# Kernel optimization log

Measured on AMD Instinct MI355X. Metric: run time of the kernel, lower is better.

The kernel has to match this reference:

```python
import jax, jax.numpy as jnp
import numpy as np

B, S, H = 1, 1024, 2048
E, F, FS = 32, 768, 4096
TOP_K = 4
SCALE = 0.02


def setup_inputs() -> dict:
    key = jax.random.key(0)
    ks = jax.random.split(key, 9)
    return {
        "hidden_states": jax.random.normal(ks[0], (B, S, H), jnp.float32),
        "router_weight": jax.random.normal(ks[1], (E, H), jnp.float32) * SCALE,
        "w_gate": jax.random.normal(ks[2], (E, H, F), jnp.float32) * SCALE,
        "w_up": jax.random.normal(ks[3], (E, H, F), jnp.float32) * SCALE,
        "w_down": jax.random.normal(ks[4], (E, F, H), jnp.float32) * SCALE,
        "sw_gate": jax.random.normal(ks[5], (H, FS), jnp.float32) * SCALE,
        "sw_up": jax.random.normal(ks[6], (H, FS), jnp.float32) * SCALE,
        "sw_down": jax.random.normal(ks[7], (FS, H), jnp.float32) * SCALE,
        "sgate_w": jax.random.normal(ks[8], (H, 1), jnp.float32) * SCALE,
    }


def reference(hidden_states, router_weight, w_gate, w_up, w_down,
              sw_gate, sw_up, sw_down, sgate_w):
    b, s, h = hidden_states.shape
    x = hidden_states.reshape(-1, h)                      # [T,H]
    T = x.shape[0]

    # ---- router: linear -> softmax (fp32) -> topk -> renormalize ----
    logits = x @ router_weight.T                          # [T,E]
    probs = jax.nn.softmax(logits.astype(jnp.float32), axis=-1)
    topv, topi = jax.lax.top_k(probs, TOP_K)              # [T,K]
    topv = topv / jnp.sum(topv, axis=-1, keepdims=True)
    topv = topv.astype(probs.dtype)

    # combine weights: scatter topk weights into dense [T,E] mask
    combine = jnp.zeros((T, E), probs.dtype).at[
        jnp.arange(T)[:, None], topi].add(topv)

    # ---- experts: SwiGLU per expert, weighted combine ----
    g = jnp.einsum('th,ehf->etf', x, w_gate)              # [E,T,F]
    u = jnp.einsum('th,ehf->etf', x, w_up)                # [E,T,F]
    act = jax.nn.silu(g) * u                              # [E,T,F]
    out = jnp.einsum('te,etf,efh->th', combine, act, w_down)  # [T,H]

    # ---- shared expert with sigmoid gate ----
    shared = (jax.nn.silu(x @ sw_gate) * (x @ sw_up)) @ sw_down  # [T,H]
    out = out + jax.nn.sigmoid(x @ sgate_w) * shared

    return out.reshape(b, s, h)
```

## Files before the change

kernel.cpp:

```cpp
#include <hip/hip_runtime.h>
#include <math.h>

#define T_TOK 1024
#define H_DIM 2048
#define N_EXP 32
#define TOPK  4
#define F_DIM 768
#define FS_DIM 4096
#define FS_HALF 2048

typedef __bf16 bf16;
typedef __attribute__((ext_vector_type(4))) __bf16 bf16x4;
typedef __attribute__((ext_vector_type(8))) __bf16 bf16x8;
typedef __attribute__((ext_vector_type(4))) float f32x4;

#define BAR() do {                                        \
    asm volatile("s_waitcnt lgkmcnt(0)" ::: "memory");    \
    __builtin_amdgcn_s_barrier();                         \
    __builtin_amdgcn_sched_barrier(0);                    \
  } while (0)

__device__ __forceinline__ int swz(int row, int colB) {
  return row * 64 + (colB ^ (((row >> 2) & 3) << 4));
}

__global__ __launch_bounds__(256) void router_kernel(
    const float* __restrict__ x, const float* __restrict__ rw,
    const float* __restrict__ sgw,
    float* __restrict__ topw, float* __restrict__ sg,
    int* __restrict__ counts, int* __restrict__ lists)
{
  int t = blockIdx.x; int tid = threadIdx.x;
  int lane = tid & 63, wave = tid >> 6;
  float acc[N_EXP];
  #pragma unroll
  for (int e = 0; e < N_EXP; e++) acc[e] = 0.f;
  float accs = 0.f;
  const float* xr = x + (size_t)t * H_DIM;
  for (int h = tid; h < H_DIM; h += 256) {
    float xv = xr[h];
    accs += xv * sgw[h];
    #pragma unroll
    for (int e = 0; e < N_EXP; e++) acc[e] += xv * rw[e * H_DIM + h];
  }
  __shared__ float red[4][N_EXP];
  __shared__ float reds[4];
  __shared__ float logits[N_EXP];
  #pragma unroll
  for (int e = 0; e < N_EXP; e++) {
    float v = acc[e];
    for (int off = 32; off; off >>= 1) v += __shfl_down(v, off, 64);
    if (lane == 0) red[wave][e] = v;
  }
  {
    float v = accs;
    for (int off = 32; off; off >>= 1) v += __shfl_down(v, off, 64);
    if (lane == 0) reds[wave] = v;
  }
  __syncthreads();
  if (tid < N_EXP) logits[tid] = red[0][tid] + red[1][tid] + red[2][tid] + red[3][tid];
  __syncthreads();
  if (tid == 0) {
    float m = -1e30f;
    #pragma unroll
    for (int e = 0; e < N_EXP; e++) m = fmaxf(m, logits[e]);
    float p[N_EXP];
    #pragma unroll
    for (int e = 0; e < N_EXP; e++) p[e] = expf(logits[e] - m);
    int ids[TOPK]; float vs[TOPK]; float wsum = 0.f;
    #pragma unroll
    for (int k = 0; k < TOPK; k++) {
      int best = 0; float bv = -1.f;
      for (int e = 0; e < N_EXP; e++) {
        if (p[e] > bv) { bv = p[e]; best = e; }
      }
      ids[k] = best; vs[k] = bv; wsum += bv; p[best] = -2.f;
    }
    float inv = 1.f / wsum;
    float sgs = reds[0] + reds[1] + reds[2] + reds[3];
    sg[t] = 1.f / (1.f + expf(-sgs));
    #pragma unroll
    for (int k = 0; k < TOPK; k++) {
      int slot = t * TOPK + k;
      topw[slot] = vs[k] * inv;
      int pos = atomicAdd(&counts[ids[k]], 1);
      lists[ids[k] * T_TOK + pos] = slot;
    }
  }
}

__global__ __launch_bounds__(256, 3) void gateup_fused(
    const float* __restrict__ X,
    const float* __restrict__ wg_, const float* __restrict__ wu_,
    const float* __restrict__ swg, const float* __restrict__ swu,
    bf16* __restrict__ act, bf16* __restrict__ acts,
    const int* __restrict__ lists, const int* __restrict__ counts,
    int n_shared, int sh_fbs, int actsN, int col_off)
{
  int id = blockIdx.x;
  bool gather = id >= n_shared;
  const float *Wg, *Wu; const int* lb = nullptr;
  int count, mt, fb, ldb, Nout; bf16* C;
  if (gather) {
    int g = id - n_shared;
    int j = g >> 3;
    int e = (g & 7) + 8 * (j / 48);
    int rr = j % 48;
    fb = (rr % 6) * 128; mt = (rr / 6) * 64;
    count = counts[e]; lb = lists + e * T_TOK;
    Wg = wg_ + (size_t)e * H_DIM * F_DIM;
    Wu = wu_ + (size_t)e * H_DIM * F_DIM;
    ldb = F_DIM; Nout = F_DIM; C = act;
  } else {
    fb = (id % sh_fbs) * 128; mt = (id / sh_fbs) * 64;
    count = T_TOK; ldb = FS_DIM; Nout = actsN;
    Wg = swg + col_off; Wu = swu + col_off;
    C = acts;
  }
  if (mt >= count) return;

  int tid = threadIdx.x;
  int lane = tid & 63, wid = tid >> 6;
  int wr = wid >> 1, wc = wid & 1;

  __shared__ alignas(16) char sA [2][64 * 64];
  __shared__ alignas(16) char sBg[2][128 * 64];
  __shared__ alignas(16) char sBu[2][128 * 64];

  const float* aptr;
  {
    int r = mt + (tid >> 2);
    int rc = r < count ? r : count - 1;
    int tok = gather ? (lb[rc] >> 2) : rc;
    aptr = X + (size_t)tok * H_DIM + ((tid & 3) << 3);
  }
  int bng = tid & 31;
  int bk4 = (tid >> 5) << 2;
  const float* bgp = Wg + (size_t)bk4 * ldb + fb + bng * 4;
  const float* bup = Wu + (size_t)bk4 * ldb + fb + bng * 4;

  f32x4 accg[2][4], accu[2][4];
  #pragma unroll
  for (int m = 0; m < 2; m++)
    #pragma unroll
    for (int n = 0; n < 4; n++) {
      accg[m][n] = (f32x4){0.f,0.f,0.f,0.f};
      accu[m][n] = (f32x4){0.f,0.f,0.f,0.f};
    }

  f32x4 av0, av1, gv[4], uv[4];

  #define ISSUE(k0) do {                                              \
    av0 = *(const f32x4*)(aptr + (k0));                               \
    av1 = *(const f32x4*)(aptr + (k0) + 4);                           \
    _Pragma("unroll")                                                 \
    for (int r_ = 0; r_ < 4; r_++) {                                  \
      gv[r_] = *(const f32x4*)(bgp + (size_t)((k0) + r_) * ldb);      \
      uv[r_] = *(const f32x4*)(bup + (size_t)((k0) + r_) * ldb);      \
    } } while (0)

  #define STAGE(b) do {                                               \
    bf16x8 t8;                                                        \
    _Pragma("unroll")                                                 \
    for (int j_ = 0; j_ < 4; j_++) {                                  \
      t8[j_] = (bf16)av0[j_]; t8[4 + j_] = (bf16)av1[j_];             \
    }                                                                 \
    *(bf16x8*)(sA[b] + swz(tid >> 2, (tid & 3) << 4)) = t8;           \
    _Pragma("unroll")                                                 \
    for (int i_ = 0; i_ < 4; i_++) {                                  \
      bf16x4 tg, tu;                                                  \
      tg[0] = (bf16)gv[0][i_]; tg[1] = (bf16)gv[1][i_];               \
      tg[2] = (bf16)gv[2][i_]; tg[3] = (bf16)gv[3][i_];               \
      tu[0] = (bf16)uv[0][i_]; tu[1] = (bf16)uv[1][i_];               \
      tu[2] = (bf16)uv[2][i_]; tu[3] = (bf16)uv[3][i_];               \
      *(bf16x4*)(sBg[b] + swz(bng * 4 + i_, bk4 << 1)) = tg;          \
      *(bf16x4*)(sBu[b] + swz(bng * 4 + i_, bk4 << 1)) = tu;          \
    } } while (0)

  #define MFMA_PHASE(b) do {                                          \
    __builtin_amdgcn_s_setprio(1);                                    \
    int l15 = lane & 15, qB = (lane >> 4) << 4;                       \
    bf16x8 af0 = *(const bf16x8*)(sA[b] + swz(wr * 32 + l15, qB));    \
    bf16x8 af1 = *(const bf16x8*)(sA[b] + swz(wr * 32 + 16 + l15, qB)); \
    _Pragma("unroll")                                                 \
    for (int n_ = 0; n_ < 4; n_++) {                                  \
      int rb = wc * 64 + n_ * 16 + l15;                               \
      bf16x8 bg = *(const bf16x8*)(sBg[b] + swz(rb, qB));             \
      bf16x8 bu = *(const bf16x8*)(sBu[b] + swz(rb, qB));             \
      accg[0][n_] = __builtin_amdgcn_mfma_f32_16x16x32_bf16(af0, bg, accg[0][n_], 0,0,0); \
      accg[1][n_] = __builtin_amdgcn_mfma_f32_16x16x32_bf16(af1, bg, accg[1][n_], 0,0,0); \
      accu[0][n_] = __builtin_amdgcn_mfma_f32_16x16x32_bf16(af0, bu, accu[0][n_], 0,0,0); \
      accu[1][n_] = __builtin_amdgcn_mfma_f32_16x16x32_bf16(af1, bu, accu[1][n_], 0,0,0); \
    }                                                                 \
    __builtin_amdgcn_s_setprio(0);                                    \
  } while (0)

  const int NT = H_DIM / 32;
  ISSUE(0);
  STAGE(0);
  ISSUE(32);
  BAR();
  for (int t = 0; t < NT - 1; ++t) {
    MFMA_PHASE(t & 1);
    STAGE((t + 1) & 1);
    if (t + 2 < NT) ISSUE((t + 2) * 32);
    BAR();
  }
  MFMA_PHASE((NT - 1) & 1);
  #undef ISSUE
  #undef STAGE
  #undef MFMA_PHASE

  #pragma unroll
  for (int m = 0; m < 2; m++) {
    #pragma unroll
    for (int q = 0; q < 4; q++) {
      int gr = mt + wr * 32 + m * 16 + (lane >> 4) * 4 + q;
      if (gr < count) {
        size_t rowo = (gather ? (size_t)lb[gr] : (size_t)gr) * Nout;
        #pragma unroll
        for (int n = 0; n < 4; n++) {
          float g = accg[m][n][q], u = accu[m][n][q];
          C[rowo + fb + wc * 64 + n * 16 + (lane & 15)] =
              (bf16)(g / (1.f + __expf(-g)) * u);
        }
      }
    }
  }
}

__global__ __launch_bounds__(256, 4) void down_fused(
    const bf16* __restrict__ act, const bf16* __restrict__ acts,
    const float* __restrict__ wd_, const float* __restrict__ swd,
    bf16* __restrict__ dslot, float* __restrict__ out,
    const float* __restrict__ sg,
    const int* __restrict__ lists, const int* __restrict__ counts,
    int n_shared, int lda_sh, int kd_sh, int swd_off, int accum)
{
  int id = blockIdx.x;
  bool expert = id >= n_shared;
  const bf16* A; const float* W; const int* lb = nullptr;
  int count, mt, nb, Kd, lda;
  if (expert) {
    int g = id - n_shared;
    int j = g >> 3;
    int e = (g & 7) + 8 * (j >> 7);
    int rr = j & 127;
    nb = (rr & 15) * 128; mt = (rr >> 4) * 64;
    count = counts[e]; lb = lists + e * T_TOK;
    A = act; lda = F_DIM; Kd = F_DIM;
    W = wd_ + (size_t)e * F_DIM * H_DIM;
  } else {
    nb = (id & 15) * 128; mt = (id >> 4) * 64;
    count = T_TOK; A = acts; lda = lda_sh; Kd = kd_sh;
    W = swd + (size_t)swd_off * H_DIM;
  }
  if (mt >= count) return;

  int tid = threadIdx.x;
  int lane = tid & 63, wid = tid >> 6;
  int wr = wid >> 1, wc = wid & 1;

  __shared__ alignas(16) char sA[2][64 * 64];
  __shared__ alignas(16) char sB[2][128 * 64];

  const bf16* aptr;
  {
    int r = mt + (tid >> 2);
    int rc = r < count ? r : count - 1;
    int ar = expert ? lb[rc] : rc;
    aptr = A + (size_t)ar * lda + ((tid & 3) << 3);
  }
  int bng = tid & 31;
  int bk4 = (tid >> 5) << 2;
  const float* bptr = W + (size_t)bk4 * H_DIM + nb + bng * 4;

  f32x4 acc[2][4];
  #pragma unroll
  for (int m = 0; m < 2; m++)
    #pragma unroll
    for (int n = 0; n < 4; n++)
      acc[m][n] = (f32x4){0.f,0.f,0.f,0.f};

  f32x4 av, bv[4];

  #define ISSUE(k0) do {                                              \
    av = *(const f32x4*)(aptr + (k0));                                \
    _Pragma("unroll")                                                 \
    for (int r_ = 0; r_ < 4; r_++)                                    \
      bv[r_] = *(const f32x4*)(bptr + (size_t)((k0) + r_) * H_DIM);   \
    } while (0)

  #define STAGE(b) do {                                               \
    *(f32x4*)(sA[b] + swz(tid >> 2, (tid & 3) << 4)) = av;            \
    _Pragma("unroll")                                                 \
    for (int i_ = 0; i_ < 4; i_++) {                                  \
      bf16x4 tb;                                                      \
      tb[0] = (bf16)bv[0][i_]; tb[1] = (bf16)bv[1][i_];               \
      tb[2] = (bf16)bv[2][i_]; tb[3] = (bf16)bv[3][i_];               \
      *(bf16x4*)(sB[b] + swz(bng * 4 + i_, bk4 << 1)) = tb;           \
    } } while (0)

  #define MFMA_PHASE(b) do {                                          \
    __builtin_amdgcn_s_setprio(1);                                    \
    int l15 = lane & 15, qB = (lane >> 4) << 4;                       \
    bf16x8 af0 = *(const bf16x8*)(sA[b] + swz(wr * 32 + l15, qB));    \
    bf16x8 af1 = *(const bf16x8*)(sA[b] + swz(wr * 32 + 16 + l15, qB)); \
    _Pragma("unroll")                                                 \
    for (int n_ = 0; n_ < 4; n_++) {                                  \
      bf16x8 bb = *(const bf16x8*)(sB[b] + swz(wc * 64 + n_ * 16 + l15, qB)); \
      acc[0][n_] = __builtin_amdgcn_mfma_f32_16x16x32_bf16(af0, bb, acc[0][n_], 0,0,0); \
      acc[1][n_] = __builtin_amdgcn_mfma_f32_16x16x32_bf16(af1, bb, acc[1][n_], 0,0,0); \
    }                                                                 \
    __builtin_amdgcn_s_setprio(0);                                    \
  } while (0)

  const int NT = Kd / 32;
  ISSUE(0);
  STAGE(0);
  ISSUE(32);
  BAR();
  for (int t = 0; t < NT - 1; ++t) {
    MFMA_PHASE(t & 1);
    STAGE((t + 1) & 1);
    if (t + 2 < NT) ISSUE((t + 2) * 32);
    BAR();
  }
  MFMA_PHASE((NT - 1) & 1);
  #undef ISSUE
  #undef STAGE
  #undef MFMA_PHASE

  #pragma unroll
  for (int m = 0; m < 2; m++) {
    #pragma unroll
    for (int q = 0; q < 4; q++) {
      int gr = mt + wr * 32 + m * 16 + (lane >> 4) * 4 + q;
      if (gr < count) {
        #pragma unroll
        for (int n = 0; n < 4; n++) {
          int col = nb + wc * 64 + n * 16 + (lane & 15);
          if (expert) {
            dslot[(size_t)lb[gr] * H_DIM + col] = (bf16)acc[m][n][q];
          } else if (!accum) {
            out[(size_t)gr * H_DIM + col] = sg[gr] * acc[m][n][q];
          } else {
            out[(size_t)gr * H_DIM + col] += sg[gr] * acc[m][n][q];
          }
        }
      }
    }
  }
}

__global__ __launch_bounds__(256) void combine_kernel(
    const bf16* __restrict__ dslot, const float* __restrict__ topw,
    float* __restrict__ out)
{
  int t = blockIdx.x;
  int h = threadIdx.x * 8;
  float w0 = topw[t * 4 + 0], w1 = topw[t * 4 + 1];
  float w2 = topw[t * 4 + 2], w3 = topw[t * 4 + 3];
  bf16x8 a0 = *(const bf16x8*)&dslot[(size_t)(t * 4 + 0) * H_DIM + h];
  bf16x8 a1 = *(const bf16x8*)&dslot[(size_t)(t * 4 + 1) * H_DIM + h];
  bf16x8 a2 = *(const bf16x8*)&dslot[(size_t)(t * 4 + 2) * H_DIM + h];
  bf16x8 a3 = *(const bf16x8*)&dslot[(size_t)(t * 4 + 3) * H_DIM + h];
  f32x4 o0 = *(f32x4*)&out[(size_t)t * H_DIM + h];
  f32x4 o1 = *(f32x4*)&out[(size_t)t * H_DIM + h + 4];
  float o[8] = {o0[0], o0[1], o0[2], o0[3], o1[0], o1[1], o1[2], o1[3]};
  #pragma unroll
  for (int j = 0; j < 8; j++)
    o[j] += w0 * (float)a0[j] + w1 * (float)a1[j] + w2 * (float)a2[j]
          + w3 * (float)a3[j];
  *(f32x4*)&out[(size_t)t * H_DIM + h]     = (f32x4){o[0], o[1], o[2], o[3]};
  *(f32x4*)&out[(size_t)t * H_DIM + h + 4] = (f32x4){o[4], o[5], o[6], o[7]};
}

extern "C" void kernel_launch(void* const* d_in, const int* in_sizes, int n_in,
                              void* d_out, int out_size, void* d_ws, size_t ws_size,
                              hipStream_t stream) {
  const float* x   = (const float*)d_in[0];
  const float* rw  = (const float*)d_in[1];
  const float* wg  = (const float*)d_in[2];
  const float* wu  = (const float*)d_in[3];
  const float* wd  = (const float*)d_in[4];
  const float* swg = (const float*)d_in[5];
  const float* swu = (const float*)d_in[6];
  const float* swd = (const float*)d_in[7];
  const float* sgw = (const float*)d_in[8];
  float* out = (float*)d_out;
  char* ws = (char*)d_ws;

  bool fullfs = ws_size >= (size_t)31700000;
  size_t actsN = fullfs ? FS_DIM : FS_HALF;

  size_t off = 0;
  int*   counts = (int*)(ws + off); off += 256;
  int*   lists  = (int*)(ws + off); off += (size_t)N_EXP * T_TOK * 4;
  float* topw   = (float*)(ws + off); off += (size_t)T_TOK * TOPK * 4;
  float* sg     = (float*)(ws + off); off += (size_t)T_TOK * 4;
  bf16*  act    = (bf16*)(ws + off); off += (size_t)T_TOK * TOPK * F_DIM * 2;
  bf16*  acts   = (bf16*)(ws + off); off += (size_t)T_TOK * actsN * 2;
  bf16*  dslot  = (bf16*)(ws + off); off += (size_t)T_TOK * TOPK * H_DIM * 2;

  hipMemsetAsync(counts, 0, 256, stream);

  router_kernel<<<T_TOK, 256, 0, stream>>>(x, rw, sgw, topw, sg, counts, lists);

  const int EXP_GU = N_EXP * 48;
  const int EXP_DN = N_EXP * 128;
  if (fullfs) {
    int nsh = 16 * (FS_DIM / 128);
    gateup_fused<<<nsh + EXP_GU, 256, 0, stream>>>(
        x, wg, wu, swg, swu, act, acts, lists, counts, nsh, FS_DIM / 128, FS_DIM, 0);
    down_fused<<<256 + EXP_DN, 256, 0, stream>>>(
        act, acts, wd, swd, dslot, out, sg, lists, counts,
        256, FS_DIM, FS_DIM, 0, 0);
  } else {
    int nsh = 16 * (FS_HALF / 128);
    gateup_fused<<<nsh + EXP_GU, 256, 0, stream>>>(
        x, wg, wu, swg, swu, act, acts, lists, counts, nsh, FS_HALF / 128, FS_HALF, 0);
    down_fused<<<256 + EXP_DN, 256, 0, stream>>>(
        act, acts, wd, swd, dslot, out, sg, lists, counts,
        256, FS_HALF, FS_HALF, 0, 0);
    gateup_fused<<<nsh, 256, 0, stream>>>(
        x, wg, wu, swg, swu, act, acts, lists, counts, nsh, FS_HALF / 128, FS_HALF, FS_HALF);
    down_fused<<<256, 256, 0, stream>>>(
        act, acts, wd, swd, dslot, out, sg, lists, counts,
        256, FS_HALF, FS_HALF, FS_HALF, 1);
  }
  combine_kernel<<<T_TOK, 256, 0, stream>>>(dslot, topw, out);
}
```

Baseline: 380.4 us.

## Add device-side work planner with persistent grid-stride MoE GEMM scheduling

Adds a planner kernel that builds compact per-expert tile lists from the routed token counts, so the gate/up and down GEMMs only visit tiles that hold real work. Until now they launched a fixed grid sized for the worst case and let empty blocks exit early. Both GEMM kernels now loop over this list with a grid stride from a fixed number of blocks. Gate/up tiles shrink from 64 to 32 rows, which cuts padding waste for experts with few tokens. The software pipeline becomes a double-register ping-pong that issues loads two stages ahead. The costs are a serial single-thread planner launch, smaller M tiles that reuse each staged weight tile across fewer rows, and more live registers.

```diff
diff --git a/kernel.cpp b/kernel.cpp
--- a/kernel.cpp
+++ b/kernel.cpp
@@ -89,139 +89,154 @@
   }
 }
 
+__global__ __launch_bounds__(64) void planner_kernel(
+    const int* __restrict__ counts, int* __restrict__ hdr,
+    int* __restrict__ gu, int* __restrict__ dn)
+{
+  if (threadIdx.x == 0) {
+    int ng = 0, nd = 0;
+    for (int e = 0; e < N_EXP; e++) {
+      int c = counts[e];
+      int mg = (c + 31) >> 5, md = (c + 63) >> 6;
+      for (int m = 0; m < mg; m++) gu[ng++] = (e << 16) | m;
+      for (int m = 0; m < md; m++) dn[nd++] = (e << 16) | m;
+    }
+    hdr[0] = ng; hdr[1] = nd;
+  }
+}
+
 __global__ __launch_bounds__(256, 3) void gateup_fused(
     const float* __restrict__ X,
     const float* __restrict__ wg_, const float* __restrict__ wu_,
     const float* __restrict__ swg, const float* __restrict__ swu,
     bf16* __restrict__ act, bf16* __restrict__ acts,
     const int* __restrict__ lists, const int* __restrict__ counts,
-    int n_shared, int sh_fbs, int actsN, int col_off)
+    const int* __restrict__ hdr, const int* __restrict__ gu_work,
+    int n_sh, int sh_nfb, int actsN, int col_off, int use_exp)
 {
-  int id = blockIdx.x;
-  bool gather = id >= n_shared;
-  const float *Wg, *Wu; const int* lb = nullptr;
-  int count, mt, fb, ldb, Nout; bf16* C;
-  if (gather) {
-    int g = id - n_shared;
-    int j = g >> 3;
-    int e = (g & 7) + 8 * (j / 48);
-    int rr = j % 48;
-    fb = (rr % 6) * 128; mt = (rr / 6) * 64;
-    count = counts[e]; lb = lists + e * T_TOK;
-    Wg = wg_ + (size_t)e * H_DIM * F_DIM;
-    Wu = wu_ + (size_t)e * H_DIM * F_DIM;
-    ldb = F_DIM; Nout = F_DIM; C = act;
-  } else {
-    fb = (id % sh_fbs) * 128; mt = (id / sh_fbs) * 64;
-    count = T_TOK; ldb = FS_DIM; Nout = actsN;
-    Wg = swg + col_off; Wu = swu + col_off;
-    C = acts;
-  }
-  if (mt >= count) return;
+  __shared__ alignas(16) char sA [2][32 * 64];
+  __shared__ alignas(16) char sBg[2][128 * 64];
+  __shared__ alignas(16) char sBu[2][128 * 64];
 
   int tid = threadIdx.x;
   int lane = tid & 63, wid = tid >> 6;
   int wr = wid >> 1, wc = wid & 1;
-
-  __shared__ alignas(16) char sA [2][64 * 64];
-  __shared__ alignas(16) char sBg[2][128 * 64];
-  __shared__ alignas(16) char sBu[2][128 * 64];
-
-  const float* aptr;
-  {
-    int r = mt + (tid >> 2);
-    int rc = r < count ? r : count - 1;
-    int tok = gather ? (lb[rc] >> 2) : rc;
-    aptr = X + (size_t)tok * H_DIM + ((tid & 3) << 3);
-  }
+  int l15 = lane & 15, qB = (lane >> 4) << 4;
   int bng = tid & 31;
   int bk4 = (tid >> 5) << 2;
-  const float* bgp = Wg + (size_t)bk4 * ldb + fb + bng * 4;
-  const float* bup = Wu + (size_t)bk4 * ldb + fb + bng * 4;
-
-  f32x4 accg[2][4], accu[2][4];
-  #pragma unroll
-  for (int m = 0; m < 2; m++)
+
+  int total = n_sh + (use_exp ? hdr[0] * 6 : 0);
+
+  for (int w = blockIdx.x; w < total; w += gridDim.x) {
+    bool gather = w >= n_sh;
+    const float *Wg, *Wu; const int* lb = nullptr;
+    int count, mt, fb, ldb, Nout; bf16* C;
+    if (gather) {
+      int r = w - n_sh;
+      int it = gu_work[r / 6];
+      int e = it >> 16;
+      mt = (it & 0xffff) * 32;
+      fb = (r % 6) * 128;
+      count = counts[e]; lb = lists + e * T_TOK;
+      Wg = wg_ + (size_t)e * H_DIM * F_DIM;
+      Wu = wu_ + (size_t)e * H_DIM * F_DIM;
+      ldb = F_DIM; Nout = F_DIM; C = act;
+    } else {
+      fb = (w % sh_nfb) * 128; mt = (w / sh_nfb) * 32;
+      count = T_TOK; ldb = FS_DIM; Nout = actsN;
+      Wg = swg + col_off; Wu = swu + col_off;
+      C = acts;
+    }
+
+    const float* aptr;
+    {
+      int r = mt + (tid >> 3);
+      int rc = r < count ? r : count - 1;
+      int tok = gather ? (lb[rc] >> 2) : rc;
+      aptr = X + (size_t)tok * H_DIM + ((tid & 7) << 2);
+    }
+    const float* bgp = Wg + (size_t)bk4 * ldb + fb + bng * 4;
+    const float* bup = Wu + (size_t)bk4 * ldb + fb + bng * 4;
+
+    f32x4 accg[4], accu[4];
     #pragma unroll
     for (int n = 0; n < 4; n++) {
-      accg[m][n] = (f32x4){0.f,0.f,0.f,0.f};
-      accu[m][n] = (f32x4){0.f,0.f,0.f,0.f};
-    }
-
-  f32x4 av0, av1, gv[4], uv[4];
-
-  #define ISSUE(k0) do {                                              \
-    av0 = *(const f32x4*)(aptr + (k0));                               \
-    av1 = *(const f32x4*)(aptr + (k0) + 4);                           \
-    _Pragma("unroll")                                                 \
-    for (int r_ = 0; r_ < 4; r_++) {                                  \
-      gv[r_] = *(const f32x4*)(bgp + (size_t)((k0) + r_) * ldb);      \
-      uv[r_] = *(const f32x4*)(bup + (size_t)((k0) + r_) * ldb);      \
-    } } while (0)
-
-  #define STAGE(b) do {                                               \
-    bf16x8 t8;                                                        \
-    _Pragma("unroll")                                                 \
-    for (int j_ = 0; j_ < 4; j_++) {                                  \
-      t8[j_] = (bf16)av0[j_]; t8[4 + j_] = (bf16)av1[j_];             \
-    }                                                                 \
-    *(bf16x8*)(sA[b] + swz(tid >> 2, (tid & 3) << 4)) = t8;           \
-    _Pragma("unroll")                                                 \
-    for (int i_ = 0; i_ < 4; i_++) {                                  \
-      bf16x4 tg, tu;                                                  \
-      tg[0] = (bf16)gv[0][i_]; tg[1] = (bf16)gv[1][i_];               \
-      tg[2] = (bf16)gv[2][i_]; tg[3] = (bf16)gv[3][i_];               \
-      tu[0] = (bf16)uv[0][i_]; tu[1] = (bf16)uv[1][i_];               \
-      tu[2] = (bf16)uv[2][i_]; tu[3] = (bf16)uv[3][i_];               \
-      *(bf16x4*)(sBg[b] + swz(bng * 4 + i_, bk4 << 1)) = tg;          \
-      *(bf16x4*)(sBu[b] + swz(bng * 4 + i_, bk4 << 1)) = tu;          \
-    } } while (0)
-
-  #define MFMA_PHASE(b) do {                                          \
-    __builtin_amdgcn_s_setprio(1);                                    \
-    int l15 = lane & 15, qB = (lane >> 4) << 4;                       \
-    bf16x8 af0 = *(const bf16x8*)(sA[b] + swz(wr * 32 + l15, qB));    \
-    bf16x8 af1 = *(const bf16x8*)(sA[b] + swz(wr * 32 + 16 + l15, qB)); \
-    _Pragma("unroll")                                                 \
-    for (int n_ = 0; n_ < 4; n_++) {                                  \
-      int rb = wc * 64 + n_ * 16 + l15;                               \
-      bf16x8 bg = *(const bf16x8*)(sBg[b] + swz(rb, qB));             \
-      bf16x8 bu = *(const bf16x8*)(sBu[b] + swz(rb, qB));             \
-      accg[0][n_] = __builtin_amdgcn_mfma_f32_16x16x32_bf16(af0, bg, accg[0][n_], 0,0,0); \
-      accg[1][n_] = __builtin_amdgcn_mfma_f32_16x16x32_bf16(af1, bg, accg[1][n_], 0,0,0); \
-      accu[0][n_] = __builtin_amdgcn_mfma_f32_16x16x32_bf16(af0, bu, accu[0][n_], 0,0,0); \
-      accu[1][n_] = __builtin_amdgcn_mfma_f32_16x16x32_bf16(af1, bu, accu[1][n_], 0,0,0); \
-    }                                                                 \
-    __builtin_amdgcn_s_setprio(0);                                    \
+      accg[n] = (f32x4){0.f,0.f,0.f,0.f};
+      accu[n] = (f32x4){0.f,0.f,0.f,0.f};
+    }
+
+    f32x4 ava, gva[4], uva[4];
+    f32x4 avb, gvb[4], uvb[4];
+
+  #define GU_ISSUE(av, gv, uv, k0) do {                               \
+      av = *(const f32x4*)(aptr + (k0));                              \
+      _Pragma("unroll")                                               \
+      for (int r_ = 0; r_ < 4; r_++) {                                \
+        gv[r_] = *(const f32x4*)(bgp + (size_t)((k0) + r_) * ldb);    \
+        uv[r_] = *(const f32x4*)(bup + (size_t)((k0) + r_) * ldb);    \
+      } } while (0)
+
+  #define GU_STAGE(b, av, gv, uv) do {                                \
+      bf16x4 ta;                                                      \
+      ta[0]=(bf16)av[0]; ta[1]=(bf16)av[1];                           \
+      ta[2]=(bf16)av[2]; ta[3]=(bf16)av[3];                           \
+      *(bf16x4*)(sA[b] + swz(tid >> 3, (tid & 7) << 3)) = ta;         \
+      _Pragma("unroll")                                               \
+      for (int i_ = 0; i_ < 4; i_++) {                                \
+        bf16x4 tg, tu;                                                \
+        tg[0]=(bf16)gv[0][i_]; tg[1]=(bf16)gv[1][i_];                 \
+        tg[2]=(bf16)gv[2][i_]; tg[3]=(bf16)gv[3][i_];                 \
+        tu[0]=(bf16)uv[0][i_]; tu[1]=(bf16)uv[1][i_];                 \
+        tu[2]=(bf16)uv[2][i_]; tu[3]=(bf16)uv[3][i_];                 \
+        *(bf16x4*)(sBg[b] + swz(bng * 4 + i_, bk4 << 1)) = tg;        \
+        *(bf16x4*)(sBu[b] + swz(bng * 4 + i_, bk4 << 1)) = tu;        \
+      } } while (0)
+
+  #define GU_MFMA(b) do {                                             \
+      __builtin_amdgcn_s_setprio(1);                                  \
+      bf16x8 af = *(const bf16x8*)(sA[b] + swz(wr * 16 + l15, qB));   \
+      _Pragma("unroll")                                               \
+      for (int n_ = 0; n_ < 4; n_++) {                                \
+        int rb = wc * 64 + n_ * 16 + l15;                             \
+        bf16x8 bg = *(const bf16x8*)(sBg[b] + swz(rb, qB));           \
+        bf16x8 bu = *(const bf16x8*)(sBu[b] + swz(rb, qB));           \
+        accg[n_] = __builtin_amdgcn_mfma_f32_16x16x32_bf16(af, bg, accg[n_], 0,0,0); \
+        accu[n_] = __builtin_amdgcn_mfma_f32_16x16x32_bf16(af, bu, accu[n_], 0,0,0); \
+      }                                                               \
+      __builtin_amdgcn_s_setprio(0);                                  \
   } while (0)
 
-  const int NT = H_DIM / 32;
-  ISSUE(0);
-  STAGE(0);
-  ISSUE(32);
-  BAR();
-  for (int t = 0; t < NT - 1; ++t) {
-    MFMA_PHASE(t & 1);
-    STAGE((t + 1) & 1);
-    if (t + 2 < NT) ISSUE((t + 2) * 32);
+    const int NT = H_DIM / 32;
+    GU_ISSUE(ava, gva, uva, 0);
+    GU_ISSUE(avb, gvb, uvb, 32);
+    GU_STAGE(0, ava, gva, uva);
+    GU_ISSUE(ava, gva, uva, 64);
     BAR();
-  }
-  MFMA_PHASE((NT - 1) & 1);
-  #undef ISSUE
-  #undef STAGE
-  #undef MFMA_PHASE
-
-  #pragma unroll
-  for (int m = 0; m < 2; m++) {
+    for (int t = 0; t < NT; t += 2) {
+      GU_MFMA(0);
+      GU_STAGE(1, avb, gvb, uvb);
+      if (t + 3 < NT) GU_ISSUE(avb, gvb, uvb, (t + 3) * 32);
+      BAR();
+      GU_MFMA(1);
+      if (t + 2 < NT) {
+        GU_STAGE(0, ava, gva, uva);
+        if (t + 4 < NT) GU_ISSUE(ava, gva, uva, (t + 4) * 32);
+      }
+      BAR();
+    }
+  #undef GU_ISSUE
+  #undef GU_STAGE
+  #undef GU_MFMA
+
     #pragma unroll
     for (int q = 0; q < 4; q++) {
-      int gr = mt + wr * 32 + m * 16 + (lane >> 4) * 4 + q;
+      int gr = mt + wr * 16 + (lane >> 4) * 4 + q;
       if (gr < count) {
         size_t rowo = (gather ? (size_t)lb[gr] : (size_t)gr) * Nout;
         #pragma unroll
         for (int n = 0; n < 4; n++) {
-          float g = accg[m][n][q], u = accu[m][n][q];
-          C[rowo + fb + wc * 64 + n * 16 + (lane & 15)] =
+          float g = accg[n][q], u = accu[n][q];
+          C[rowo + fb + wc * 64 + n * 16 + l15] =
               (bf16)(g / (1.f + __expf(-g)) * u);
         }
       }
@@ -235,117 +250,126 @@
     bf16* __restrict__ dslot, float* __restrict__ out,
     const float* __restrict__ sg,
     const int* __restrict__ lists, const int* __restrict__ counts,
-    int n_shared, int lda_sh, int kd_sh, int swd_off, int accum)
+    const int* __restrict__ hdr, const int* __restrict__ dn_work,
+    int n_sh, int lda_sh, int kd_sh, int swd_off, int accum, int use_exp)
 {
-  int id = blockIdx.x;
-  bool expert = id >= n_shared;
-  const bf16* A; const float* W; const int* lb = nullptr;
-  int count, mt, nb, Kd, lda;
-  if (expert) {
-    int g = id - n_shared;
-    int j = g >> 3;
-    int e = (g & 7) + 8 * (j >> 7);
-    int rr = j & 127;
-    nb = (rr & 15) * 128; mt = (rr >> 4) * 64;
-    count = counts[e]; lb = lists + e * T_TOK;
-    A = act; lda = F_DIM; Kd = F_DIM;
-    W = wd_ + (size_t)e * F_DIM * H_DIM;
-  } else {
-    nb = (id & 15) * 128; mt = (id >> 4) * 64;
-    count = T_TOK; A = acts; lda = lda_sh; Kd = kd_sh;
-    W = swd + (size_t)swd_off * H_DIM;
-  }
-  if (mt >= count) return;
+  __shared__ alignas(16) char sA[2][64 * 64];
+  __shared__ alignas(16) char sB[2][128 * 64];
 
   int tid = threadIdx.x;
   int lane = tid & 63, wid = tid >> 6;
   int wr = wid >> 1, wc = wid & 1;
-
-  __shared__ alignas(16) char sA[2][64 * 64];
-  __shared__ alignas(16) char sB[2][128 * 64];
-
-  const bf16* aptr;
-  {
-    int r = mt + (tid >> 2);
-    int rc = r < count ? r : count - 1;
-    int ar = expert ? lb[rc] : rc;
-    aptr = A + (size_t)ar * lda + ((tid & 3) << 3);
-  }
+  int l15 = lane & 15, qB = (lane >> 4) << 4;
   int bng = tid & 31;
   int bk4 = (tid >> 5) << 2;
-  const float* bptr = W + (size_t)bk4 * H_DIM + nb + bng * 4;
-
-  f32x4 acc[2][4];
-  #pragma unroll
-  for (int m = 0; m < 2; m++)
-    #pragma unroll
-    for (int n = 0; n < 4; n++)
-      acc[m][n] = (f32x4){0.f,0.f,0.f,0.f};
-
-  f32x4 av, bv[4];
-
-  #define ISSUE(k0) do {                                              \
-    av = *(const f32x4*)(aptr + (k0));                                \
-    _Pragma("unroll")                                                 \
-    for (int r_ = 0; r_ < 4; r_++)                                    \
-      bv[r_] = *(const f32x4*)(bptr + (size_t)((k0) + r_) * H_DIM);   \
-    } while (0)
-
-  #define STAGE(b) do {                                               \
-    *(f32x4*)(sA[b] + swz(tid >> 2, (tid & 3) << 4)) = av;            \
-    _Pragma("unroll")                                                 \
-    for (int i_ = 0; i_ < 4; i_++) {                                  \
-      bf16x4 tb;                                                      \
-      tb[0] = (bf16)bv[0][i_]; tb[1] = (bf16)bv[1][i_];               \
-      tb[2] = (bf16)bv[2][i_]; tb[3] = (bf16)bv[3][i_];               \
-      *(bf16x4*)(sB[b] + swz(bng * 4 + i_, bk4 << 1)) = tb;           \
-    } } while (0)
-
-  #define MFMA_PHASE(b) do {                                          \
-    __builtin_amdgcn_s_setprio(1);                                    \
-    int l15 = lane & 15, qB = (lane >> 4) << 4;                       \
-    bf16x8 af0 = *(const bf16x8*)(sA[b] + swz(wr * 32 + l15, qB));    \
-    bf16x8 af1 = *(const bf16x8*)(sA[b] + swz(wr * 32 + 16 + l15, qB)); \
-    _Pragma("unroll")                                                 \
-    for (int n_ = 0; n_ < 4; n_++) {                                  \
-      bf16x8 bb = *(const bf16x8*)(sB[b] + swz(wc * 64 + n_ * 16 + l15, qB)); \
-      acc[0][n_] = __builtin_amdgcn_mfma_f32_16x16x32_bf16(af0, bb, acc[0][n_], 0,0,0); \
-      acc[1][n_] = __builtin_amdgcn_mfma_f32_16x16x32_bf16(af1, bb, acc[1][n_], 0,0,0); \
-    }                                                                 \
-    __builtin_amdgcn_s_setprio(0);                                    \
+
+  int total = n_sh + (use_exp ? hdr[1] * 16 : 0);
+
+  for (int w = blockIdx.x; w < total; w += gridDim.x) {
+    bool expert = w >= n_sh;
+    const bf16* A; const float* W; const int* lb = nullptr;
+    int count, mt, nb, Kd, lda;
+    if (expert) {
+      int r = w - n_sh;
+      int it = dn_work[r >> 4];
+      int e = it >> 16;
+      mt = (it & 0xffff) * 64;
+      nb = (r & 15) * 128;
+      count = counts[e]; lb = lists + e * T_TOK;
+      A = act; lda = F_DIM; Kd = F_DIM;
+      W = wd_ + (size_t)e * F_DIM * H_DIM;
+    } else {
+      nb = (w & 15) * 128; mt = (w >> 4) * 64;
+      count = T_TOK; A = acts; lda = lda_sh; Kd = kd_sh;
+      W = swd + (size_t)swd_off * H_DIM;
+    }
+
+    const bf16* aptr;
+    {
+      int r = mt + (tid >> 2);
+      int rc = r < count ? r : count - 1;
+      int ar = expert ? lb[rc] : rc;
+      aptr = A + (size_t)ar * lda + ((tid & 3) << 3);
+    }
+    const float* bptr = W + (size_t)bk4 * H_DIM + nb + bng * 4;
+
+    f32x4 acc[2][4];
+    #pragma unroll
+    for (int m = 0; m < 2; m++)
+      #pragma unroll
+      for (int n = 0; n < 4; n++)
+        acc[m][n] = (f32x4){0.f,0.f,0.f,0.f};
+
+    uint4 ava, avb; f32x4 bva[4], bvb[4];
+
+  #define DN_ISSUE(av, bv, k0) do {                                   \
+      av = *(const uint4*)(aptr + (k0));                              \
+      _Pragma("unroll")                                               \
+      for (int r_ = 0; r_ < 4; r_++)                                  \
+        bv[r_] = *(const f32x4*)(bptr + (size_t)((k0) + r_) * H_DIM); \
+      } while (0)
+
+  #define DN_STAGE(b, av, bv) do {                                    \
+      *(uint4*)(sA[b] + swz(tid >> 2, (tid & 3) << 4)) = av;          \
+      _Pragma("unroll")                                               \
+      for (int i_ = 0; i_ < 4; i_++) {                                \
+        bf16x4 tb;                                                    \
+        tb[0]=(bf16)bv[0][i_]; tb[1]=(bf16)bv[1][i_];                 \
+        tb[2]=(bf16)bv[2][i_]; tb[3]=(bf16)bv[3][i_];                 \
+        *(bf16x4*)(sB[b] + swz(bng * 4 + i_, bk4 << 1)) = tb;         \
+      } } while (0)
+
+  #define DN_MFMA(b) do {                                             \
+      __builtin_amdgcn_s_setprio(1);                                  \
+      bf16x8 af0 = *(const bf16x8*)(sA[b] + swz(wr * 32 + l15, qB));  \
+      bf16x8 af1 = *(const bf16x8*)(sA[b] + swz(wr * 32 + 16 + l15, qB)); \
+      _Pragma("unroll")                                               \
+      for (int n_ = 0; n_ < 4; n_++) {                                \
+        bf16x8 bb = *(const bf16x8*)(sB[b] + swz(wc * 64 + n_ * 16 + l15, qB)); \
+        acc[0][n_] = __builtin_amdgcn_mfma_f32_16x16x32_bf16(af0, bb, acc[0][n_], 0,0,0); \
+        acc[1][n_] = __builtin_amdgcn_mfma_f32_16x16x32_bf16(af1, bb, acc[1][n_], 0,0,0); \
+      }                                                               \
+      __builtin_amdgcn_s_setprio(0);                                  \
   } while (0)
 
-  const int NT = Kd / 32;
-  ISSUE(0);
-  STAGE(0);
-  ISSUE(32);
-  BAR();
-  for (int t = 0; t < NT - 1; ++t) {
-    MFMA_PHASE(t & 1);
-    STAGE((t + 1) & 1);
-    if (t + 2 < NT) ISSUE((t + 2) * 32);
+    const int NT = Kd / 32;
+    DN_ISSUE(ava, bva, 0);
+    DN_ISSUE(avb, bvb, 32);
+    DN_STAGE(0, ava, bva);
+    DN_ISSUE(ava, bva, 64);
     BAR();
-  }
-  MFMA_PHASE((NT - 1) & 1);
-  #undef ISSUE
-  #undef STAGE
-  #undef MFMA_PHASE
-
-  #pragma unroll
-  for (int m = 0; m < 2; m++) {
-    #pragma unroll
-    for (int q = 0; q < 4; q++) {
-      int gr = mt + wr * 32 + m * 16 + (lane >> 4) * 4 + q;
-      if (gr < count) {
-        #pragma unroll
-        for (int n = 0; n < 4; n++) {
-          int col = nb + wc * 64 + n * 16 + (lane & 15);
-          if (expert) {
-            dslot[(size_t)lb[gr] * H_DIM + col] = (bf16)acc[m][n][q];
-          } else if (!accum) {
-            out[(size_t)gr * H_DIM + col] = sg[gr] * acc[m][n][q];
-          } else {
-            out[(size_t)gr * H_DIM + col] += sg[gr] * acc[m][n][q];
+    for (int t = 0; t < NT; t += 2) {
+      DN_MFMA(0);
+      DN_STAGE(1, avb, bvb);
+      if (t + 3 < NT) DN_ISSUE(avb, bvb, (t + 3) * 32);
+      BAR();
+      DN_MFMA(1);
+      if (t + 2 < NT) {
+        DN_STAGE(0, ava, bva);
+        if (t + 4 < NT) DN_ISSUE(ava, bva, (t + 4) * 32);
+      }
+      BAR();
+    }
+  #undef DN_ISSUE
+  #undef DN_STAGE
+  #undef DN_MFMA
+
+    #pragma unroll
+    for (int m = 0; m < 2; m++) {
+      #pragma unroll
+      for (int q = 0; q < 4; q++) {
+        int gr = mt + wr * 32 + m * 16 + (lane >> 4) * 4 + q;
+        if (gr < count) {
+          #pragma unroll
+          for (int n = 0; n < 4; n++) {
+            int col = nb + wc * 64 + n * 16 + l15;
+            if (expert) {
+              dslot[(size_t)lb[gr] * H_DIM + col] = (bf16)acc[m][n][q];
+            } else if (!accum) {
+              out[(size_t)gr * H_DIM + col] = sg[gr] * acc[m][n][q];
+            } else {
+              out[(size_t)gr * H_DIM + col] += sg[gr] * acc[m][n][q];
+            }
           }
         }
       }
@@ -395,39 +419,44 @@
   size_t actsN = fullfs ? FS_DIM : FS_HALF;
 
   size_t off = 0;
-  int*   counts = (int*)(ws + off); off += 256;
-  int*   lists  = (int*)(ws + off); off += (size_t)N_EXP * T_TOK * 4;
-  float* topw   = (float*)(ws + off); off += (size_t)T_TOK * TOPK * 4;
-  float* sg     = (float*)(ws + off); off += (size_t)T_TOK * 4;
-  bf16*  act    = (bf16*)(ws + off); off += (size_t)T_TOK * TOPK * F_DIM * 2;
-  bf16*  acts   = (bf16*)(ws + off); off += (size_t)T_TOK * actsN * 2;
-  bf16*  dslot  = (bf16*)(ws + off); off += (size_t)T_TOK * TOPK * H_DIM * 2;
+  int*   counts  = (int*)(ws + off); off += 256;
+  int*   hdr     = (int*)(ws + off); off += 64;
+  int*   gu_work = (int*)(ws + off); off += 4096;
+  int*   dn_work = (int*)(ws + off); off += 2048;
+  int*   lists   = (int*)(ws + off); off += (size_t)N_EXP * T_TOK * 4;
+  float* topw    = (float*)(ws + off); off += (size_t)T_TOK * TOPK * 4;
+  float* sg      = (float*)(ws + off); off += (size_t)T_TOK * 4;
+  bf16*  act     = (bf16*)(ws + off); off += (size_t)T_TOK * TOPK * F_DIM * 2;
+  bf16*  acts    = (bf16*)(ws + off); off += (size_t)T_TOK * actsN * 2;
+  bf16*  dslot   = (bf16*)(ws + off); off += (size_t)T_TOK * TOPK * H_DIM * 2;
 
   hipMemsetAsync(counts, 0, 256, stream);
 
   router_kernel<<<T_TOK, 256, 0, stream>>>(x, rw, sgw, topw, sg, counts, lists);
-
-  const int EXP_GU = N_EXP * 48;
-  const int EXP_DN = N_EXP * 128;
+  planner_kernel<<<1, 64, 0, stream>>>(counts, hdr, gu_work, dn_work);
+
   if (fullfs) {
-    int nsh = 16 * (FS_DIM / 128);
-    gateup_fused<<<nsh + EXP_GU, 256, 0, stream>>>(
-        x, wg, wu, swg, swu, act, acts, lists, counts, nsh, FS_DIM / 128, FS_DIM, 0);
-    down_fused<<<256 + EXP_DN, 256, 0, stream>>>(
-        act, acts, wd, swd, dslot, out, sg, lists, counts,
-        256, FS_DIM, FS_DIM, 0, 0);
+    int nsh_gu = 32 * (FS_DIM / 128);
+    gateup_fused<<<768, 256, 0, stream>>>(
+        x, wg, wu, swg, swu, act, acts, lists, counts, hdr, gu_work,
+        nsh_gu, FS_DIM / 128, FS_DIM, 0, 1);
+    down_fused<<<1024, 256, 0, stream>>>(
+        act, acts, wd, swd, dslot, out, sg, lists, counts, hdr, dn_work,
+        256, FS_DIM, FS_DIM, 0, 0, 1);
   } else {
-    int nsh = 16 * (FS_HALF / 128);
-    gateup_fused<<<nsh + EXP_GU, 256, 0, stream>>>(
-        x, wg, wu, swg, swu, act, acts, lists, counts, nsh, FS_HALF / 128, FS_HALF, 0);
-    down_fused<<<256 + EXP_DN, 256, 0, stream>>>(
-        act, acts, wd, swd, dslot, out, sg, lists, counts,
-        256, FS_HALF, FS_HALF, 0, 0);
-    gateup_fused<<<nsh, 256, 0, stream>>>(
-        x, wg, wu, swg, swu, act, acts, lists, counts, nsh, FS_HALF / 128, FS_HALF, FS_HALF);
+    int nsh_gu = 32 * (FS_HALF / 128);
+    gateup_fused<<<768, 256, 0, stream>>>(
+        x, wg, wu, swg, swu, act, acts, lists, counts, hdr, gu_work,
+        nsh_gu, FS_HALF / 128, FS_HALF, 0, 1);
+    down_fused<<<1024, 256, 0, stream>>>(
+        act, acts, wd, swd, dslot, out, sg, lists, counts, hdr, dn_work,
+        256, FS_HALF, FS_HALF, 0, 0, 1);
+    gateup_fused<<<512, 256, 0, stream>>>(
+        x, wg, wu, swg, swu, act, acts, lists, counts, hdr, gu_work,
+        nsh_gu, FS_HALF / 128, FS_HALF, FS_HALF, 0);
     down_fused<<<256, 256, 0, stream>>>(
-        act, acts, wd, swd, dslot, out, sg, lists, counts,
-        256, FS_HALF, FS_HALF, FS_HALF, 1);
+        act, acts, wd, swd, dslot, out, sg, lists, counts, hdr, dn_work,
+        256, FS_HALF, FS_HALF, FS_HALF, 1, 0);
   }
   combine_kernel<<<T_TOK, 256, 0, stream>>>(dslot, topw, out);
 }
```

Result: slower. 552.0 us (+45.1%).
